# Kernel optimization log

Hardware: AMD Instinct MI355X
Metric: run time of the kernel (lower is better)

The kernel has to match this reference:

```python
import jax, jax.numpy as jnp
import numpy as np

HID = 256
EDGE_F = 64
N_CELL = 4096
N_EDGE = 65536
BSZ = 4
EPS = 1e-5


def setup_inputs() -> dict:
    key = jax.random.key(0)
    ks = jax.random.split(key, 12)
    def lin(k, fan_in, fan_out):
        # torch Linear default init: U(-1/sqrt(fan_in), 1/sqrt(fan_in))
        bound = 1.0 / np.sqrt(fan_in)
        kw, kb = jax.random.split(k)
        W = jax.random.uniform(kw, (fan_in, fan_out), jnp.float32, -bound, bound)
        b = jax.random.uniform(kb, (fan_out,), jnp.float32, -bound, bound)
        return W, b
    cell_x = jax.random.normal(ks[0], (BSZ, N_CELL, HID), jnp.float32)
    edge_index = jax.random.randint(ks[1], (BSZ, N_EDGE, 2), 0, N_CELL, jnp.int64)
    edge_attr = jax.random.normal(ks[2], (BSZ, N_EDGE, EDGE_F), jnp.float32)
    mW1, mb1 = lin(ks[3], HID + EDGE_F, HID)
    mW2, mb2 = lin(ks[4], HID, HID)
    uW1, ub1 = lin(ks[5], 2 * HID, HID)
    uW2, ub2 = lin(ks[6], HID, HID)
    gamma = jnp.ones((HID,), jnp.float32)
    beta = jnp.zeros((HID,), jnp.float32)
    return {"cell_x": cell_x, "edge_index": edge_index, "edge_attr": edge_attr,
            "mW1": mW1, "mb1": mb1, "mW2": mW2, "mb2": mb2,
            "uW1": uW1, "ub1": ub1, "uW2": uW2, "ub2": ub2,
            "gamma": gamma, "beta": beta}


def reference(cell_x, edge_index, edge_attr, mW1, mb1, mW2, mb2,
              uW1, ub1, uW2, ub2, gamma, beta):
    n_cell = cell_x.shape[1]
    src = jnp.clip(edge_index[..., 0], 0, n_cell - 1)  # [B, E]
    dst = jnp.clip(edge_index[..., 1], 0, n_cell - 1)  # [B, E]

    # gather source node features per edge: [B, E, H]
    src_x = jnp.take_along_axis(cell_x, src[..., None], axis=1)

    # edge message MLP
    m_in = jnp.concatenate([src_x, edge_attr], axis=-1)  # [B, E, H+F]
    msg = jax.nn.relu(m_in @ mW1 + mb1) @ mW2 + mb2      # [B, E, H]

    # mean aggregation at destination nodes (scatter-add + count)
    def agg_one(m, d):
        s = jax.ops.segment_sum(m, d, num_segments=n_cell)                    # [N, H]
        c = jax.ops.segment_sum(jnp.ones((d.shape[0],), m.dtype), d,
                                num_segments=n_cell)                          # [N]
        return s / jnp.maximum(c, 1.0)[:, None]
    agg = jax.vmap(agg_one)(msg, dst)  # [B, N, H]

    # node update MLP + residual LayerNorm
    u_in = jnp.concatenate([cell_x, agg], axis=-1)        # [B, N, 2H]
    out = jax.nn.relu(u_in @ uW1 + ub1) @ uW2 + ub2       # [B, N, H]
    h = cell_x + out
    mu = jnp.mean(h, axis=-1, keepdims=True)
    var = jnp.mean(jnp.square(h - mu), axis=-1, keepdims=True)
    return (h - mu) * jax.lax.rsqrt(var + EPS) * gamma + beta
```

## Files before the change

kernel.cpp:

```cpp
#include <hip/hip_runtime.h>

#define HID 256
#define EF  64
#define KIN 320
#define NC  4096
#define NE  65536
#define BSZ 4
#define EPSV 1e-5f

typedef unsigned short ushort_t;
typedef __attribute__((ext_vector_type(8))) short s16x8;
typedef __attribute__((ext_vector_type(16))) float f32x16;

#define EPAD 68
#define HPAD 260
#define UPAD 520
#define HSF  260

__device__ __forceinline__ ushort_t bf16_rne(float f) {
    unsigned u = __float_as_uint(f);
    return (ushort_t)((u + 0x7fffu + ((u >> 16) & 1u)) >> 16);
}
__device__ __forceinline__ float bf16_to_f(ushort_t u) {
    return __uint_as_float(((unsigned)u) << 16);
}
__device__ __forceinline__ void split_bf16(float v, ushort_t& h, ushort_t& l) {
    unsigned u = __float_as_uint(v);
    h = (ushort_t)(u >> 16);
    float hf = __uint_as_float(u & 0xffff0000u);
    l = (ushort_t)(__float_as_uint(v - hf) >> 16);
}

__device__ __forceinline__ void pack_one(const float* W, int idx,
                                         ushort_t* hi, ushort_t* lo) {
    int l = idx & 63;
    int tn = idx >> 6;
    int nt = tn & 7, t = tn >> 3;
    int k0 = t * 16 + (l >> 5) * 8;
    int col = nt * 32 + (l & 31);
    #pragma unroll
    for (int j = 0; j < 8; ++j) {
        float v = W[(size_t)(k0 + j) * 256 + col];
        ushort_t h, lw;
        split_bf16(v, h, lw);
        hi[(size_t)idx * 8 + j] = h;
        lo[(size_t)idx * 8 + j] = lw;
    }
}

#define FR1 10240
#define FR2 8192
#define PACK1B 104
#define FUSEB 256
#define ZEROB 256

__global__ __launch_bounds__(256)
void prep_kernel(const float* __restrict__ mW1, const float* __restrict__ uW1,
                 const float* __restrict__ uW2, const float* __restrict__ mW2,
                 const float* __restrict__ ub1, const float* __restrict__ mb2,
                 ushort_t* __restrict__ w1hi, ushort_t* __restrict__ w1lo,
                 ushort_t* __restrict__ u1hi, ushort_t* __restrict__ u1lo,
                 ushort_t* __restrict__ u2hi, ushort_t* __restrict__ u2lo,
                 float* __restrict__ W2u, float* __restrict__ bias2u,
                 float4* __restrict__ zp, int n4) {
    int bid = blockIdx.x;
    if (bid < PACK1B) {
        int idx = bid * 256 + threadIdx.x;
        if (idx < FR1) { pack_one(mW1, idx, w1hi, w1lo); return; }
        idx -= FR1;
        if (idx < FR2) { pack_one(uW1, idx, u1hi, u1lo); return; }
        idx -= FR2;
        pack_one(uW2, idx, u2hi, u2lo);
        return;
    }
    bid -= PACK1B;
    if (bid < FUSEB) {
        int k = bid, n = threadIdx.x;
        const float* wrow = mW2 + (size_t)k * 256;
        float acc = 0.f;
        #pragma unroll 8
        for (int m = 0; m < 256; ++m)
            acc = fmaf(wrow[m], uW1[(size_t)(256 + m) * 256 + n], acc);
        W2u[(size_t)k * 256 + n] = acc;
        return;
    }
    bid -= FUSEB;
    if (bid == 0) {
        int n = threadIdx.x;
        float acc = ub1[n];
        #pragma unroll 8
        for (int m = 0; m < 256; ++m)
            acc = fmaf(mb2[m], uW1[(size_t)(256 + m) * 256 + n], acc);
        bias2u[n] = acc;
        return;
    }
    bid -= 1;
    int i = bid * 256 + threadIdx.x;
    int stride = ZEROB * 256;
    float4 z = make_float4(0.f, 0.f, 0.f, 0.f);
    for (; i < n4; i += stride) zp[i] = z;
}

__global__ __launch_bounds__(256)
void hist_kernel(const int* __restrict__ eidx, float* __restrict__ counts) {
    int i = blockIdx.x * 256 + threadIdx.x;
    int b = i >> 16;
    int2 v = ((const int2*)eidx)[i];
    int d = min(max(v.y, 0), NC - 1);
    atomicAdd(&counts[b * NC + d], 1.0f);
}

__global__ __launch_bounds__(1024)
void scan_kernel(const float* __restrict__ counts, int* __restrict__ woff,
                 const float* __restrict__ W2u,
                 ushort_t* __restrict__ w2uhi, ushort_t* __restrict__ w2ulo) {
    if (blockIdx.x >= BSZ) {
        if (threadIdx.x < 256) {
            int idx = (blockIdx.x - BSZ) * 256 + threadIdx.x;
            pack_one(W2u, idx, w2uhi, w2ulo);
        }
        return;
    }
    __shared__ int wsum[16];
    int b = blockIdx.x, t = threadIdx.x;
    int base = b * NC + t * 4;
    int v0 = (int)counts[base],     v1 = (int)counts[base + 1];
    int v2 = (int)counts[base + 2], v3 = (int)counts[base + 3];
    int ts = v0 + v1 + v2 + v3;
    int lane = t & 63;
    int x = ts;
    #pragma unroll
    for (int off = 1; off < 64; off <<= 1) {
        int y = __shfl_up(x, off, 64);
        if (lane >= off) x += y;
    }
    if (lane == 63) wsum[t >> 6] = x;
    __syncthreads();
    if (t == 0) {
        int s = 0;
        #pragma unroll
        for (int w = 0; w < 16; ++w) { int tmp = wsum[w]; wsum[w] = s; s += tmp; }
    }
    __syncthreads();
    int excl = wsum[t >> 6] + (x - ts);
    woff[base]     = excl;
    woff[base + 1] = excl + v0;
    woff[base + 2] = excl + v0 + v1;
    woff[base + 3] = excl + v0 + v1 + v2;
}

__global__ __launch_bounds__(512, 4)
void sp_kernel(const int* __restrict__ eidx, int* __restrict__ woff,
               int* __restrict__ sorted,
               const float* __restrict__ cell_x,
               const ushort_t* __restrict__ w1hi, const ushort_t* __restrict__ w1lo,
               const ushort_t* __restrict__ u1hi, const ushort_t* __restrict__ u1lo,
               float* __restrict__ Pe, ushort_t* __restrict__ Pn) {
    __shared__ ushort_t Us[32 * HPAD];

    if (blockIdx.x < 512) {
        int i = blockIdx.x * 512 + threadIdx.x;
        int b = i >> 16, e = i & (NE - 1);
        int2 v = ((const int2*)eidx)[i];
        int d = min(max(v.y, 0), NC - 1);
        int pos = atomicAdd(&woff[b * NC + d], 1);
        sorted[(size_t)b * NE + pos] = e;
        return;
    }

    const int tid = threadIdx.x;
    const size_t r0 = (size_t)(blockIdx.x - 512) * 32;
    const int wv = tid >> 6, ln = tid & 63;
    const int m32 = ln & 31, half = ln >> 5;
    const int col = wv * 32 + m32;

    const ushort_t* wph = w1hi + ((size_t)wv * 64 + ln) * 8;
    const ushort_t* wpl = w1lo + ((size_t)wv * 64 + ln) * 8;
    const ushort_t* uph = u1hi + ((size_t)wv * 64 + ln) * 8;
    const ushort_t* upl = u1lo + ((size_t)wv * 64 + ln) * 8;
    s16x8 wh = *(const s16x8*)wph, wl = *(const s16x8*)wpl;
    s16x8 uh = *(const s16x8*)uph, ul = *(const s16x8*)upl;

    {
        const int row = tid >> 4, c8 = tid & 15;
        const float4* crow = (const float4*)(cell_x + (r0 + row) * HID);
        #pragma unroll
        for (int i = 0; i < 4; ++i) {
            int c = c8 + i * 16;
            float4 v = crow[c];
            *(ushort4*)&Us[row * HPAD + c * 4] =
                make_ushort4(bf16_rne(v.x), bf16_rne(v.y), bf16_rne(v.z), bf16_rne(v.w));
        }
    }
    __syncthreads();

    f32x16 aw, au;
    #pragma unroll
    for (int r = 0; r < 16; ++r) { aw[r] = 0.f; au[r] = 0.f; }

    #pragma unroll 2
    for (int t = 0; t < 16; ++t) {
        int tn = (t + 1 < 16) ? t + 1 : 15;
        s16x8 whn = *(const s16x8*)(wph + (size_t)tn * 4096);
        s16x8 wln = *(const s16x8*)(wpl + (size_t)tn * 4096);
        s16x8 uhn = *(const s16x8*)(uph + (size_t)tn * 4096);
        s16x8 uln = *(const s16x8*)(upl + (size_t)tn * 4096);
        s16x8 a = *(const s16x8*)&Us[m32 * HPAD + t * 16 + half * 8];
        aw = __builtin_amdgcn_mfma_f32_32x32x16_bf16(a, wh, aw, 0, 0, 0);
        aw = __builtin_amdgcn_mfma_f32_32x32x16_bf16(a, wl, aw, 0, 0, 0);
        au = __builtin_amdgcn_mfma_f32_32x32x16_bf16(a, uh, au, 0, 0, 0);
        au = __builtin_amdgcn_mfma_f32_32x32x16_bf16(a, ul, au, 0, 0, 0);
        wh = whn; wl = wln; uh = uhn; ul = uln;
    }

    #pragma unroll
    for (int r = 0; r < 16; ++r) {
        int row = (r & 3) + 8 * (r >> 2) + 4 * half;
        Pe[(r0 + row) * 256 + col] = aw[r];
        Pn[(r0 + row) * 256 + col] = bf16_rne(au[r]);
    }
}

__global__ __launch_bounds__(512, 4)
void edge_kernel(const float* __restrict__ Pe,
                 const int*   __restrict__ eidx,
                 const int*   __restrict__ sorted,
                 const float* __restrict__ eattr,
                 const ushort_t* __restrict__ w1hi, const ushort_t* __restrict__ w1lo,
                 const float* __restrict__ b1,
                 float* __restrict__ aggf) {
    __shared__ ushort_t Xs[64 * EPAD];

    const int tid = threadIdx.x;
    const int b   = blockIdx.x >> 10;
    const int e0  = (blockIdx.x & 1023) * 64;
    const int wv = tid >> 6, ln = tid & 63;
    const int m32 = ln & 31, half = ln >> 5;
    const int col = wv * 32 + m32;

    int eid = sorted[(size_t)b * NE + e0 + ln];
    int2 ev = ((const int2*)eidx)[(size_t)b * NE + eid];
    int src = min(max(ev.x, 0), NC - 1);
    int dst = min(max(ev.y, 0), NC - 1);

    const ushort_t* ph = w1hi + ((size_t)(16 * 8 + wv) * 64 + ln) * 8;
    const ushort_t* pl = w1lo + ((size_t)(16 * 8 + wv) * 64 + ln) * 8;
    s16x8 bh0 = *(const s16x8*)ph;
    s16x8 bl0 = *(const s16x8*)pl;
    s16x8 bh1 = *(const s16x8*)(ph + 4096);
    s16x8 bl1 = *(const s16x8*)(pl + 4096);
    s16x8 bh2 = *(const s16x8*)(ph + 8192);
    s16x8 bl2 = *(const s16x8*)(pl + 8192);
    s16x8 bh3 = *(const s16x8*)(ph + 12288);
    s16x8 bl3 = *(const s16x8*)(pl + 12288);

    float t0[16], t1[16];
    {
        const float* pb = Pe + (size_t)b * NC * 256 + col;
        #pragma unroll
        for (int r = 0; r < 16; ++r) {
            int rw = (r & 3) + 8 * (r >> 2) + 4 * half;
            t0[r] = pb[(size_t)__shfl(src, rw, 64) * 256];
            t1[r] = pb[(size_t)__shfl(src, rw + 32, 64) * 256];
        }
    }

    {
        const int rowE = tid >> 3, c8 = tid & 7;
        int eidr = __shfl(eid, rowE, 64);
        const float4* arow = (const float4*)(eattr + ((size_t)b * NE + eidr) * EF);
        #pragma unroll
        for (int i = 0; i < 2; ++i) {
            int c = c8 + i * 8;
            float4 v = arow[c];
            *(ushort4*)&Xs[rowE * EPAD + c * 4] =
                make_ushort4(bf16_rne(v.x), bf16_rne(v.y), bf16_rne(v.z), bf16_rne(v.w));
        }
    }
    __syncthreads();

    f32x16 A0, A1;
    {
        float bias = b1[col];
        #pragma unroll
        for (int r = 0; r < 16; ++r) { A0[r] = bias; A1[r] = bias; }
    }
    {
        int ao = m32 * EPAD + half * 8;
        s16x8 a0, a1;
        a0 = *(const s16x8*)&Xs[ao];      a1 = *(const s16x8*)&Xs[ao + 32 * EPAD];
        A0 = __builtin_amdgcn_mfma_f32_32x32x16_bf16(a0, bh0, A0, 0, 0, 0);
        A0 = __builtin_amdgcn_mfma_f32_32x32x16_bf16(a0, bl0, A0, 0, 0, 0);
        A1 = __builtin_amdgcn_mfma_f32_32x32x16_bf16(a1, bh0, A1, 0, 0, 0);
        A1 = __builtin_amdgcn_mfma_f32_32x32x16_bf16(a1, bl0, A1, 0, 0, 0);
        a0 = *(const s16x8*)&Xs[ao + 16]; a1 = *(const s16x8*)&Xs[ao + 16 + 32 * EPAD];
        A0 = __builtin_amdgcn_mfma_f32_32x32x16_bf16(a0, bh1, A0, 0, 0, 0);
        A0 = __builtin_amdgcn_mfma_f32_32x32x16_bf16(a0, bl1, A0, 0, 0, 0);
        A1 = __builtin_amdgcn_mfma_f32_32x32x16_bf16(a1, bh1, A1, 0, 0, 0);
        A1 = __builtin_amdgcn_mfma_f32_32x32x16_bf16(a1, bl1, A1, 0, 0, 0);
        a0 = *(const s16x8*)&Xs[ao + 32]; a1 = *(const s16x8*)&Xs[ao + 32 + 32 * EPAD];
        A0 = __builtin_amdgcn_mfma_f32_32x32x16_bf16(a0, bh2, A0, 0, 0, 0);
        A0 = __builtin_amdgcn_mfma_f32_32x32x16_bf16(a0, bl2, A0, 0, 0, 0);
        A1 = __builtin_amdgcn_mfma_f32_32x32x16_bf16(a1, bh2, A1, 0, 0, 0);
        A1 = __builtin_amdgcn_mfma_f32_32x32x16_bf16(a1, bl2, A1, 0, 0, 0);
        a0 = *(const s16x8*)&Xs[ao + 48]; a1 = *(const s16x8*)&Xs[ao + 48 + 32 * EPAD];
        A0 = __builtin_amdgcn_mfma_f32_32x32x16_bf16(a0, bh3, A0, 0, 0, 0);
        A0 = __builtin_amdgcn_mfma_f32_32x32x16_bf16(a0, bl3, A0, 0, 0, 0);
        A1 = __builtin_amdgcn_mfma_f32_32x32x16_bf16(a1, bh3, A1, 0, 0, 0);
        A1 = __builtin_amdgcn_mfma_f32_32x32x16_bf16(a1, bl3, A1, 0, 0, 0);
    }

    #pragma unroll
    for (int r = 0; r < 16; ++r) {
        A0[r] = fmaxf(A0[r] + t0[r], 0.f);
        A1[r] = fmaxf(A1[r] + t1[r], 0.f);
    }

    {
        const int l31 = ln & 31;
        int dl = __shfl(dst, l31, 64);
        int dp = __shfl(dst, (l31 == 0) ? 0 : l31 - 1, 64);
        if (l31 == 0) dp = ~dl;
        unsigned m = (unsigned)__ballot(dl != dp);
        unsigned rem = m & ~1u;
        int lo = 0;
        while (lo < 32) {
            int hi = rem ? (int)__builtin_ctz(rem) : 32;
            rem &= rem - 1;
            int d = __shfl(dl, lo, 64);
            float s = 0.f;
            #pragma unroll
            for (int r = 0; r < 16; ++r) {
                int row = (r & 3) + 8 * (r >> 2) + 4 * half;
                s += (row >= lo && row < hi) ? A0[r] : 0.f;
            }
            s += __shfl_xor(s, 32, 64);
            if (ln < 32) atomicAdd(&aggf[((size_t)b * NC + d) * HID + col], s);
            lo = hi;
        }
        dl = __shfl(dst, 32 + l31, 64);
        dp = __shfl(dst, 32 + ((l31 == 0) ? 0 : l31 - 1), 64);
        if (l31 == 0) dp = ~dl;
        m = (unsigned)__ballot(dl != dp);
        rem = m & ~1u;
        lo = 0;
        while (lo < 32) {
            int hi = rem ? (int)__builtin_ctz(rem) : 32;
            rem &= rem - 1;
            int d = __shfl(dl, lo, 64);
            float s = 0.f;
            #pragma unroll
            for (int r = 0; r < 16; ++r) {
                int row = (r & 3) + 8 * (r >> 2) + 4 * half;
                s += (row >= lo && row < hi) ? A1[r] : 0.f;
            }
            s += __shfl_xor(s, 32, 64);
            if (ln < 32) atomicAdd(&aggf[((size_t)b * NC + d) * HID + col], s);
            lo = hi;
        }
    }
}

__global__ __launch_bounds__(512, 6)
void node_kernel(const float* __restrict__ cell_x,
                 const float* __restrict__ aggf,
                 const float* __restrict__ counts,
                 const ushort_t* __restrict__ Pn,
                 const ushort_t* __restrict__ w2uhi, const ushort_t* __restrict__ w2ulo,
                 const float* __restrict__ bias2u,
                 const ushort_t* __restrict__ u2hi, const ushort_t* __restrict__ u2lo,
                 const float* __restrict__ b2,
                 const float* __restrict__ gamma, const float* __restrict__ beta,
                 float* __restrict__ out) {
    __shared__ ushort_t Us[32 * UPAD];
    float* hs = (float*)Us;

    const int tid = threadIdx.x;
    const int b   = blockIdx.x >> 7;
    const int r0  = (blockIdx.x & 127) * 32;
    const int wv = tid >> 6, ln = tid & 63;
    const int m32 = ln & 31, half = ln >> 5;
    const int col = wv * 32 + m32;

    const ushort_t* b1ph = w2uhi + ((size_t)wv * 64 + ln) * 8;
    const ushort_t* b1pl = w2ulo + ((size_t)wv * 64 + ln) * 8;
    s16x8 bhi = *(const s16x8*)b1ph;
    s16x8 blo = *(const s16x8*)b1pl;

    ushort_t pnt[16];
    {
        const ushort_t* pb = Pn + ((size_t)b * NC + r0) * 256 + col;
        #pragma unroll
        for (int r = 0; r < 16; ++r) {
            int row = (r & 3) + 8 * (r >> 2) + 4 * half;
            pnt[r] = pb[(size_t)row * 256];
        }
    }

    {
        const int row = tid >> 4, c8 = tid & 15;
        float inv = 1.0f / fmaxf(counts[b * NC + r0 + row], 1.0f);
        const float4* grow = (const float4*)(aggf + ((size_t)b * NC + r0 + row) * HID);
        #pragma unroll
        for (int i = 0; i < 4; ++i) {
            int c = c8 + i * 16;
            float4 g = grow[c];
            *(ushort4*)&Us[row * HPAD + c * 4] =
                make_ushort4(bf16_rne(g.x * inv), bf16_rne(g.y * inv),
                             bf16_rne(g.z * inv), bf16_rne(g.w * inv));
        }
    }
    __syncthreads();

    f32x16 acc;
    {
        float bias = bias2u[col];
        #pragma unroll
        for (int r = 0; r < 16; ++r) acc[r] = bias;
    }
    #pragma unroll 2
    for (int t = 0; t < 16; ++t) {
        int tn1 = (t + 1 < 16) ? t + 1 : 15;
        s16x8 bhin = *(const s16x8*)(b1ph + (size_t)tn1 * 4096);
        s16x8 blon = *(const s16x8*)(b1pl + (size_t)tn1 * 4096);
        s16x8 a = *(const s16x8*)&Us[m32 * HPAD + t * 16 + half * 8];
        acc = __builtin_amdgcn_mfma_f32_32x32x16_bf16(a, bhi, acc, 0, 0, 0);
        acc = __builtin_amdgcn_mfma_f32_32x32x16_bf16(a, blo, acc, 0, 0, 0);
        bhi = bhin; blo = blon;
    }

    #pragma unroll
    for (int r = 0; r < 16; ++r) acc[r] += bf16_to_f(pnt[r]);

    const ushort_t* b2ph = u2hi + ((size_t)wv * 64 + ln) * 8;
    const ushort_t* b2pl = u2lo + ((size_t)wv * 64 + ln) * 8;
    bhi = *(const s16x8*)b2ph;
    blo = *(const s16x8*)b2pl;

    __syncthreads();

    #pragma unroll
    for (int r = 0; r < 16; ++r) {
        int row = (r & 3) + 8 * (r >> 2) + 4 * half;
        Us[row * HPAD + col] = bf16_rne(fmaxf(acc[r], 0.f));
    }
    __syncthreads();

    float cxt[16];
    #pragma unroll
    for (int r = 0; r < 16; ++r) {
        int row = (r & 3) + 8 * (r >> 2) + 4 * half;
        cxt[r] = cell_x[((size_t)b * NC + r0 + row) * HID + col];
    }

    f32x16 c2;
    {
        float bias = b2[col];
        #pragma unroll
        for (int r = 0; r < 16; ++r) c2[r] = bias;
    }
    #pragma unroll 2
    for (int t = 0; t < 16; ++t) {
        int tn1 = (t + 1 < 16) ? t + 1 : 15;
        s16x8 bhin = *(const s16x8*)(b2ph + (size_t)tn1 * 4096);
        s16x8 blon = *(const s16x8*)(b2pl + (size_t)tn1 * 4096);
        s16x8 a = *(const s16x8*)&Us[m32 * HPAD + t * 16 + half * 8];
        c2 = __builtin_amdgcn_mfma_f32_32x32x16_bf16(a, bhi, c2, 0, 0, 0);
        c2 = __builtin_amdgcn_mfma_f32_32x32x16_bf16(a, blo, c2, 0, 0, 0);
        bhi = bhin; blo = blon;
    }
    __syncthreads();

    #pragma unroll
    for (int r = 0; r < 16; ++r) {
        int row = (r & 3) + 8 * (r >> 2) + 4 * half;
        hs[row * HSF + col] = c2[r] + cxt[r];
    }
    __syncthreads();

    #pragma unroll
    for (int i = 0; i < 4; ++i) {
        int r = wv * 4 + i;
        float v[4];
        float s = 0.f, q = 0.f;
        #pragma unroll
        for (int j = 0; j < 4; ++j) {
            v[j] = hs[r * HSF + ln + 64 * j];
            s += v[j];
            q = fmaf(v[j], v[j], q);
        }
        #pragma unroll
        for (int off = 32; off > 0; off >>= 1) {
            s += __shfl_xor(s, off, 64);
            q += __shfl_xor(q, off, 64);
        }
        float mu = s * (1.0f / HID);
        float var = q * (1.0f / HID) - mu * mu;
        float rs = rsqrtf(var + EPSV);
        float* orow = out + ((size_t)b * NC + r0 + r) * HID;
        #pragma unroll
        for (int j = 0; j < 4; ++j) {
            int c = ln + 64 * j;
            orow[c] = (v[j] - mu) * rs * gamma[c] + beta[c];
        }
    }
}

extern "C" void kernel_launch(void* const* d_in, const int* in_sizes, int n_in,
                              void* d_out, int out_size, void* d_ws, size_t ws_size,
                              hipStream_t stream) {
    const float* cell_x = (const float*)d_in[0];
    const int*   eidx   = (const int*)d_in[1];
    const float* eattr  = (const float*)d_in[2];
    const float* mW1    = (const float*)d_in[3];
    const float* mb1    = (const float*)d_in[4];
    const float* mW2    = (const float*)d_in[5];
    const float* mb2    = (const float*)d_in[6];
    const float* uW1    = (const float*)d_in[7];
    const float* ub1    = (const float*)d_in[8];
    const float* uW2    = (const float*)d_in[9];
    const float* ub2    = (const float*)d_in[10];
    const float* gamma  = (const float*)d_in[11];
    const float* beta   = (const float*)d_in[12];
    float* out = (float*)d_out;

    float* aggf   = (float*)d_ws;
    float* counts = aggf + (size_t)BSZ * NC * HID;
    int*   woff   = (int*)(counts + BSZ * NC);
    int*   sorted = woff + BSZ * NC;
    ushort_t* w1hi = (ushort_t*)(sorted + (size_t)BSZ * NE);
    ushort_t* w1lo = w1hi + KIN * HID;
    ushort_t* u1hi = w1lo + KIN * HID;
    ushort_t* u1lo = u1hi + HID * HID;
    ushort_t* u2hi = u1lo + HID * HID;
    ushort_t* u2lo = u2hi + HID * HID;
    ushort_t* w2uhi = u2lo + HID * HID;
    ushort_t* w2ulo = w2uhi + HID * HID;
    float*    W2u   = (float*)(w2ulo + HID * HID);
    float*    bias2u = W2u + HID * HID;
    float*    Pe   = bias2u + HID;
    ushort_t* Pn   = (ushort_t*)(Pe + (size_t)BSZ * NC * 256);

    int n4 = (BSZ * NC * HID * 4 + BSZ * NC * 4) / 16;
    prep_kernel<<<PACK1B + FUSEB + 1 + ZEROB, 256, 0, stream>>>(
        mW1, uW1, uW2, mW2, ub1, mb2,
        w1hi, w1lo, u1hi, u1lo, u2hi, u2lo, W2u, bias2u, (float4*)d_ws, n4);
    hist_kernel<<<BSZ * NE / 256, 256, 0, stream>>>(eidx, counts);
    scan_kernel<<<BSZ + 32, 1024, 0, stream>>>(counts, woff, W2u, w2uhi, w2ulo);
    sp_kernel<<<512 + BSZ * NC / 32, 512, 0, stream>>>(eidx, woff, sorted, cell_x,
                                                       w1hi, w1lo, u1hi, u1lo, Pe, Pn);
    edge_kernel<<<BSZ * NE / 64, 512, 0, stream>>>(Pe, eidx, sorted, eattr,
                                                   w1hi, w1lo, mb1, aggf);
    node_kernel<<<BSZ * NC / 32, 512, 0, stream>>>(cell_x, aggf, counts, Pn,
                                                   w2uhi, w2ulo, bias2u,
                                                   u2hi, u2lo, ub2,
                                                   gamma, beta, out);
}
```

Baseline: 257.2 us.

## Merge histogram, scan and scatter into fewer kernels; use packed bf16 conversion

Folds the destination histogram and the W2u packing into the projection kernel. The exclusive scan is recomputed per block in shared memory inside a new scan-plus-scatter kernel, which replaces three small launches with two. The aim is to cut launch gaps and serialization between tiny kernels. It adds a separate 'filled' counter array that must be zeroed, redundant scan work in each of 512 blocks, and swaps the manual bf16 rounding for packed __float22bfloat162_rn conversions.

```diff
diff --git a/kernel.cpp b/kernel.cpp
--- a/kernel.cpp
+++ b/kernel.cpp
@@ -1,4 +1,5 @@
 #include <hip/hip_runtime.h>
+#include <hip/hip_bf16.h>
 
 #define HID 256
 #define EF  64
@@ -23,6 +24,10 @@
 }
 __device__ __forceinline__ float bf16_to_f(ushort_t u) {
     return __uint_as_float(((unsigned)u) << 16);
+}
+__device__ __forceinline__ unsigned pk_bf16(float a, float b) {
+    __hip_bfloat162 h = __float22bfloat162_rn(make_float2(a, b));
+    return *reinterpret_cast<unsigned*>(&h);
 }
 __device__ __forceinline__ void split_bf16(float v, ushort_t& h, ushort_t& l) {
     unsigned u = __float_as_uint(v);
@@ -101,70 +106,27 @@
     for (; i < n4; i += stride) zp[i] = z;
 }
 
-__global__ __launch_bounds__(256)
-void hist_kernel(const int* __restrict__ eidx, float* __restrict__ counts) {
-    int i = blockIdx.x * 256 + threadIdx.x;
-    int b = i >> 16;
-    int2 v = ((const int2*)eidx)[i];
-    int d = min(max(v.y, 0), NC - 1);
-    atomicAdd(&counts[b * NC + d], 1.0f);
-}
-
-__global__ __launch_bounds__(1024)
-void scan_kernel(const float* __restrict__ counts, int* __restrict__ woff,
-                 const float* __restrict__ W2u,
-                 ushort_t* __restrict__ w2uhi, ushort_t* __restrict__ w2ulo) {
-    if (blockIdx.x >= BSZ) {
-        if (threadIdx.x < 256) {
-            int idx = (blockIdx.x - BSZ) * 256 + threadIdx.x;
-            pack_one(W2u, idx, w2uhi, w2ulo);
-        }
-        return;
-    }
-    __shared__ int wsum[16];
-    int b = blockIdx.x, t = threadIdx.x;
-    int base = b * NC + t * 4;
-    int v0 = (int)counts[base],     v1 = (int)counts[base + 1];
-    int v2 = (int)counts[base + 2], v3 = (int)counts[base + 3];
-    int ts = v0 + v1 + v2 + v3;
-    int lane = t & 63;
-    int x = ts;
-    #pragma unroll
-    for (int off = 1; off < 64; off <<= 1) {
-        int y = __shfl_up(x, off, 64);
-        if (lane >= off) x += y;
-    }
-    if (lane == 63) wsum[t >> 6] = x;
-    __syncthreads();
-    if (t == 0) {
-        int s = 0;
-        #pragma unroll
-        for (int w = 0; w < 16; ++w) { int tmp = wsum[w]; wsum[w] = s; s += tmp; }
-    }
-    __syncthreads();
-    int excl = wsum[t >> 6] + (x - ts);
-    woff[base]     = excl;
-    woff[base + 1] = excl + v0;
-    woff[base + 2] = excl + v0 + v1;
-    woff[base + 3] = excl + v0 + v1 + v2;
-}
-
 __global__ __launch_bounds__(512, 4)
-void sp_kernel(const int* __restrict__ eidx, int* __restrict__ woff,
-               int* __restrict__ sorted,
+void hp_kernel(const int* __restrict__ eidx, float* __restrict__ counts,
                const float* __restrict__ cell_x,
                const ushort_t* __restrict__ w1hi, const ushort_t* __restrict__ w1lo,
                const ushort_t* __restrict__ u1hi, const ushort_t* __restrict__ u1lo,
-               float* __restrict__ Pe, ushort_t* __restrict__ Pn) {
+               float* __restrict__ Pe, ushort_t* __restrict__ Pn,
+               const float* __restrict__ W2u,
+               ushort_t* __restrict__ w2uhi, ushort_t* __restrict__ w2ulo) {
     __shared__ ushort_t Us[32 * HPAD];
 
     if (blockIdx.x < 512) {
         int i = blockIdx.x * 512 + threadIdx.x;
-        int b = i >> 16, e = i & (NE - 1);
+        int b = i >> 16;
         int2 v = ((const int2*)eidx)[i];
         int d = min(max(v.y, 0), NC - 1);
-        int pos = atomicAdd(&woff[b * NC + d], 1);
-        sorted[(size_t)b * NE + pos] = e;
+        atomicAdd(&counts[b * NC + d], 1.0f);
+        return;
+    }
+    if (blockIdx.x >= 1024) {
+        int idx = (blockIdx.x - 1024) * 512 + threadIdx.x;
+        pack_one(W2u, idx, w2uhi, w2ulo);
         return;
     }
 
@@ -188,8 +150,8 @@
         for (int i = 0; i < 4; ++i) {
             int c = c8 + i * 16;
             float4 v = crow[c];
-            *(ushort4*)&Us[row * HPAD + c * 4] =
-                make_ushort4(bf16_rne(v.x), bf16_rne(v.y), bf16_rne(v.z), bf16_rne(v.w));
+            *(uint2*)&Us[row * HPAD + c * 4] =
+                make_uint2(pk_bf16(v.x, v.y), pk_bf16(v.z, v.w));
         }
     }
     __syncthreads();
@@ -222,6 +184,48 @@
 }
 
 __global__ __launch_bounds__(512, 4)
+void scansc_kernel(const int* __restrict__ eidx, const float* __restrict__ counts,
+                   int* __restrict__ filled, int* __restrict__ sorted) {
+    __shared__ int woffL[NC];
+    __shared__ int wsum[8];
+
+    const int t = threadIdx.x;
+    const int b = blockIdx.x >> 7;
+
+    int c[8];
+    int ts = 0;
+    const int base = b * NC + t * 8;
+    #pragma unroll
+    for (int j = 0; j < 8; ++j) { c[j] = (int)counts[base + j]; ts += c[j]; }
+
+    int lane = t & 63;
+    int x = ts;
+    #pragma unroll
+    for (int off = 1; off < 64; off <<= 1) {
+        int y = __shfl_up(x, off, 64);
+        if (lane >= off) x += y;
+    }
+    if (lane == 63) wsum[t >> 6] = x;
+    __syncthreads();
+    if (t == 0) {
+        int s = 0;
+        #pragma unroll
+        for (int w = 0; w < 8; ++w) { int tmp = wsum[w]; wsum[w] = s; s += tmp; }
+    }
+    __syncthreads();
+    int run = wsum[t >> 6] + (x - ts);
+    #pragma unroll
+    for (int j = 0; j < 8; ++j) { woffL[t * 8 + j] = run; run += c[j]; }
+    __syncthreads();
+
+    int e = (blockIdx.x & 127) * 512 + t;
+    int2 v = ((const int2*)eidx)[(size_t)b * NE + e];
+    int d = min(max(v.y, 0), NC - 1);
+    int pos = woffL[d] + atomicAdd(&filled[b * NC + d], 1);
+    sorted[(size_t)b * NE + pos] = e;
+}
+
+__global__ __launch_bounds__(512, 4)
 void edge_kernel(const float* __restrict__ Pe,
                  const int*   __restrict__ eidx,
                  const int*   __restrict__ sorted,
@@ -273,8 +277,8 @@
         for (int i = 0; i < 2; ++i) {
             int c = c8 + i * 8;
             float4 v = arow[c];
-            *(ushort4*)&Xs[rowE * EPAD + c * 4] =
-                make_ushort4(bf16_rne(v.x), bf16_rne(v.y), bf16_rne(v.z), bf16_rne(v.w));
+            *(uint2*)&Xs[rowE * EPAD + c * 4] =
+                make_uint2(pk_bf16(v.x, v.y), pk_bf16(v.z, v.w));
         }
     }
     __syncthreads();
@@ -405,9 +409,8 @@
         for (int i = 0; i < 4; ++i) {
             int c = c8 + i * 16;
             float4 g = grow[c];
-            *(ushort4*)&Us[row * HPAD + c * 4] =
-                make_ushort4(bf16_rne(g.x * inv), bf16_rne(g.y * inv),
-                             bf16_rne(g.z * inv), bf16_rne(g.w * inv));
+            *(uint2*)&Us[row * HPAD + c * 4] =
+                make_uint2(pk_bf16(g.x * inv, g.y * inv), pk_bf16(g.z * inv, g.w * inv));
         }
     }
     __syncthreads();
@@ -526,8 +529,8 @@
 
     float* aggf   = (float*)d_ws;
     float* counts = aggf + (size_t)BSZ * NC * HID;
-    int*   woff   = (int*)(counts + BSZ * NC);
-    int*   sorted = woff + BSZ * NC;
+    int*   filled = (int*)(counts + BSZ * NC);
+    int*   sorted = filled + BSZ * NC;
     ushort_t* w1hi = (ushort_t*)(sorted + (size_t)BSZ * NE);
     ushort_t* w1lo = w1hi + KIN * HID;
     ushort_t* u1hi = w1lo + KIN * HID;
@@ -541,14 +544,14 @@
     float*    Pe   = bias2u + HID;
     ushort_t* Pn   = (ushort_t*)(Pe + (size_t)BSZ * NC * 256);
 
-    int n4 = (BSZ * NC * HID * 4 + BSZ * NC * 4) / 16;
+    int n4 = (BSZ * NC * HID * 4 + BSZ * NC * 4 + BSZ * NC * 4) / 16;
     prep_kernel<<<PACK1B + FUSEB + 1 + ZEROB, 256, 0, stream>>>(
         mW1, uW1, uW2, mW2, ub1, mb2,
         w1hi, w1lo, u1hi, u1lo, u2hi, u2lo, W2u, bias2u, (float4*)d_ws, n4);
-    hist_kernel<<<BSZ * NE / 256, 256, 0, stream>>>(eidx, counts);
-    scan_kernel<<<BSZ + 32, 1024, 0, stream>>>(counts, woff, W2u, w2uhi, w2ulo);
-    sp_kernel<<<512 + BSZ * NC / 32, 512, 0, stream>>>(eidx, woff, sorted, cell_x,
-                                                       w1hi, w1lo, u1hi, u1lo, Pe, Pn);
+    hp_kernel<<<1040, 512, 0, stream>>>(eidx, counts, cell_x,
+                                        w1hi, w1lo, u1hi, u1lo, Pe, Pn,
+                                        W2u, w2uhi, w2ulo);
+    scansc_kernel<<<512, 512, 0, stream>>>(eidx, counts, filled, sorted);
     edge_kernel<<<BSZ * NE / 64, 512, 0, stream>>>(Pe, eidx, sorted, eattr,
                                                    w1hi, w1lo, mb1, aggf);
     node_kernel<<<BSZ * NC / 32, 512, 0, stream>>>(cell_x, aggf, counts, Pn,
```

Measured after the change: 255.5 us. About the same (-0.7%).
